# Kernel optimization log

Measured on AMD Instinct MI355X. Metric: run time of the kernel, lower is better.

Reference implementation:

```python
import jax, jax.numpy as jnp
import numpy as np

B, S, F_IN, D, H, DFF, L = 64, 256, 64, 512, 8, 2048, 6
A_DIM, FEAT, OUT = 8, 32, 5
EPS = 1e-3  # keras default epsilon for BatchNorm/LayerNorm


def _sinusoidal_pes(seq_len, d_model):
    pos = np.arange(seq_len)[:, None].astype(np.float32)
    i = np.arange(d_model)[None, :].astype(np.float32)
    angle = pos / np.power(10000.0, (2.0 * np.floor(i / 2.0)) / d_model)
    pe = np.zeros((seq_len, d_model), dtype=np.float32)
    pe[:, 0::2] = np.sin(angle[:, 0::2])
    pe[:, 1::2] = np.cos(angle[:, 1::2])
    return jnp.asarray(pe)


def setup_inputs() -> dict:
    key = jax.random.key(0)
    ks = jax.random.split(key, 16)
    w = lambda k, shape: 0.02 * jax.random.normal(k, shape, dtype=jnp.float32)
    return {
        'state': jax.random.normal(ks[0], (B, S, F_IN), dtype=jnp.float32),
        'action': jax.random.normal(ks[1], (B, A_DIM), dtype=jnp.float32),
        'pes': _sinusoidal_pes(S, D),
        'W_emb': w(ks[2], (F_IN, D)), 'b_emb': jnp.zeros((D,), jnp.float32),
        'Wq': w(ks[3], (L, D, D)), 'bq': jnp.zeros((L, D), jnp.float32),
        'Wk': w(ks[4], (L, D, D)), 'bk': jnp.zeros((L, D), jnp.float32),
        'Wv': w(ks[5], (L, D, D)), 'bv': jnp.zeros((L, D), jnp.float32),
        'Wo': w(ks[6], (L, D, D)), 'bo': jnp.zeros((L, D), jnp.float32),
        'bn_gamma': jnp.ones((L, D), jnp.float32), 'bn_beta': jnp.zeros((L, D), jnp.float32),
        'W1': w(ks[7], (L, D, DFF)), 'b1': jnp.zeros((L, DFF), jnp.float32),
        'W2': w(ks[8], (L, DFF, D)), 'b2': jnp.zeros((L, D), jnp.float32),
        'ln_gamma': jnp.ones((L, D), jnp.float32), 'ln_beta': jnp.zeros((L, D), jnp.float32),
        'Wf': w(ks[9], (S * D, FEAT)), 'bf': jnp.zeros((FEAT,), jnp.float32),
        'Wfin': w(ks[10], (FEAT + A_DIM, OUT)), 'bfin': jnp.zeros((OUT,), jnp.float32),
    }


def _encoder(x, pes, layer_params):
    # x: [B, S, D]
    x = x + pes  # positional encoding

    def step(h, p):
        Wq, bq, Wk, bk, Wv, bv, Wo, bo, gb, bb, W1, b1, W2, b2, gl, bl = p
        b, s, d = h.shape
        dh = d // H
        q = (h @ Wq + bq).reshape(b, s, H, dh)
        k = (h @ Wk + bk).reshape(b, s, H, dh)
        v = (h @ Wv + bv).reshape(b, s, H, dh)
        scores = jnp.einsum('bqhd,bkhd->bhqk', q, k) / jnp.sqrt(jnp.asarray(dh, h.dtype))
        attn = jax.nn.softmax(scores, axis=-1)
        ctx = jnp.einsum('bhqk,bkhd->bqhd', attn, v).reshape(b, s, d)
        ctx = ctx @ Wo + bo
        y = h + ctx
        # BatchNormalization over (batch, seq), per-channel (training-mode batch stats)
        mu = y.mean(axis=(0, 1))
        var = y.var(axis=(0, 1))
        y = gb * (y - mu) * jax.lax.rsqrt(var + EPS) + bb
        # FFN + residual + LayerNorm
        f = jax.nn.relu(y @ W1 + b1) @ W2 + b2
        z = y + f
        mu2 = z.mean(axis=-1, keepdims=True)
        var2 = z.var(axis=-1, keepdims=True)
        z = gl * (z - mu2) * jax.lax.rsqrt(var2 + EPS) + bl
        return z, None

    x, _ = jax.lax.scan(step, x, layer_params)
    return x


def reference(state, action, pes, W_emb, b_emb, Wq, bq, Wk, bk, Wv, bv, Wo, bo,
              bn_gamma, bn_beta, W1, b1, W2, b2, ln_gamma, ln_beta, Wf, bf, Wfin, bfin):
    x = state @ W_emb + b_emb                       # [B, S, D]
    layer_params = (Wq, bq, Wk, bk, Wv, bv, Wo, bo, bn_gamma, bn_beta,
                    W1, b1, W2, b2, ln_gamma, ln_beta)
    enc = _encoder(x, pes, layer_params)            # [B, S, D]
    flat = enc.reshape(enc.shape[0], -1)            # [B, S*D]
    feat = flat @ Wf + bf                           # [B, 32]
    out = jnp.concatenate([feat, action], axis=-1) @ Wfin + bfin  # [B, 5]
    return out
```

## Files before the change

kernel.cpp:

```cpp
#include <hip/hip_runtime.h>

typedef short bf16x8 __attribute__((ext_vector_type(8)));
typedef float f32x4 __attribute__((ext_vector_type(4)));
typedef unsigned short us;

#define BN_EPS 1e-3f

static __device__ __forceinline__ us f2bs(float x) {
  unsigned int u = __builtin_bit_cast(unsigned int, x);
  unsigned int r = (u + 0x7FFFu + ((u >> 16) & 1u)) >> 16;
  return (us)r;
}
static __device__ __forceinline__ float b2f(us v) {
  unsigned int u = (unsigned int)v << 16;
  return __builtin_bit_cast(float, u);
}

static __device__ __forceinline__ void gl_lds16(const us* g, us* l) {
  __builtin_amdgcn_global_load_lds(
      (const __attribute__((address_space(1))) void*)g,
      (__attribute__((address_space(3))) void*)l, 16, 0, 0);
}

__global__ __launch_bounds__(256) void transpose_bf16(
    const float* __restrict__ src, us* __restrict__ dst, int K, int N,
    long sstride, long dstride) {
  long sbs = (long)blockIdx.z * sstride;
  long sbd = (long)blockIdx.z * dstride;
  __shared__ float tile[32][33];
  int tx = threadIdx.x & 31, ty = threadIdx.x >> 5;
  int k0 = blockIdx.x * 32, n0 = blockIdx.y * 32;
  for (int i = 0; i < 32; i += 8)
    tile[ty + i][tx] = src[sbs + (long)(k0 + ty + i) * N + n0 + tx];
  __syncthreads();
  for (int i = 0; i < 32; i += 8)
    dst[sbd + (long)(n0 + ty + i) * K + k0 + tx] = f2bs(tile[tx][ty + i]);
}

__global__ __launch_bounds__(256) void embed_kernel(
    const float* __restrict__ state, const float* __restrict__ Wemb,
    const float* __restrict__ bemb, const float* __restrict__ pes,
    us* __restrict__ hb) {
  int t = threadIdx.x;
  int row0 = blockIdx.x * 8;
  __shared__ float st[8][64];
  {
    int i = t;
    st[i >> 6][i & 63] = state[(long)row0 * 64 + i];
    i += 256;
    st[i >> 6][i & 63] = state[(long)row0 * 64 + i];
  }
  __syncthreads();
  int c0 = t, c1 = t + 256;
  float acc0[8], acc1[8];
#pragma unroll
  for (int r = 0; r < 8; ++r) { acc0[r] = 0.f; acc1[r] = 0.f; }
  for (int kk = 0; kk < 64; ++kk) {
    float w0 = Wemb[kk * 512 + c0], w1 = Wemb[kk * 512 + c1];
#pragma unroll
    for (int r = 0; r < 8; ++r) {
      acc0[r] += st[r][kk] * w0;
      acc1[r] += st[r][kk] * w1;
    }
  }
  float be0 = bemb[c0], be1 = bemb[c1];
#pragma unroll
  for (int r = 0; r < 8; ++r) {
    int row = row0 + r, s = row & 255;
    hb[(long)row * 512 + c0] = f2bs(acc0[r] + be0 + pes[(long)s * 512 + c0]);
    hb[(long)row * 512 + c1] = f2bs(acc1[r] + be1 + pes[(long)s * 512 + c1]);
  }
}

enum { EPI_QKV = 0, EPI_RESID_BF16 = 1, EPI_RELU_BF16 = 2, EPI_FFN2_BF16 = 3,
       EPI_FEAT = 4 };

template <int EPI>
__global__ __launch_bounds__(512, 2) void gemm256(
    const us* __restrict__ A, int lda, const us* __restrict__ Bt, int ldb,
    void* __restrict__ Cout, void* __restrict__ C2, void* __restrict__ C3,
    int ldc, const float* __restrict__ bias, const us* __restrict__ resid,
    const float* __restrict__ gamma, const float* __restrict__ beta, int K) {
  const int tid = threadIdx.x;
  const int w = tid >> 6, l = tid & 63;
  const int wr = w >> 2, wc = w & 3;
  const int lr = l & 15, lh = l >> 4;
  const long m0 = (long)blockIdx.x * 256;
  const long n0 = (long)blockIdx.y * 256;
  const int KC = K >> 5;
  __shared__ __align__(16) us sh[4 * 16384];
  const int o = tid * 16;
  const int lg = o ^ ((o >> 2) & 0x30);
  const int sr = lg >> 6;
  const int sc = (lg & 63) >> 1;
  const int pb = lr * 32 + ((lh * 8) ^ ((lr & 3) << 3));
  const us* Asl = sh + wr * 4096 + pb;
  const us* Bsl = sh + 8192 + (wc >> 1) * 4096 + (wc & 1) * 2048 + pb;

  for (int j = 0; j < 3; ++j) {
    us* slot = sh + j * 16384;
    gl_lds16(A + (m0 + sr) * lda + j * 32 + sc, slot + tid * 8);
    gl_lds16(A + (m0 + 128 + sr) * lda + j * 32 + sc, slot + 4096 + tid * 8);
    gl_lds16(Bt + (n0 + sr) * ldb + j * 32 + sc, slot + 8192 + tid * 8);
    gl_lds16(Bt + (n0 + 128 + sr) * ldb + j * 32 + sc, slot + 12288 + tid * 8);
  }
  asm volatile("s_waitcnt vmcnt(8)" ::: "memory");
  __builtin_amdgcn_s_barrier();

  f32x4 acc[8][4] = {};
  for (int c = 0; c < KC; ++c) {
    const int soff = (c & 3) * 16384;
    const bool st = (c + 3) < KC;
    us* nslot = sh + ((c + 3) & 3) * 16384;
    const int nk = (c + 3) * 32;
    if (st) {
      gl_lds16(A + (m0 + sr) * lda + nk + sc, nslot + tid * 8);
      gl_lds16(A + (m0 + 128 + sr) * lda + nk + sc, nslot + 4096 + tid * 8);
    }
    bf16x8 bfr[4], af[4];
#pragma unroll
    for (int ni = 0; ni < 4; ++ni)
      bfr[ni] = *(const bf16x8*)(Bsl + soff + ni * 512);
#pragma unroll
    for (int mi = 0; mi < 4; ++mi)
      af[mi] = *(const bf16x8*)(Asl + soff + mi * 512);
    __builtin_amdgcn_s_barrier();
    __builtin_amdgcn_s_setprio(1);
#pragma unroll
    for (int mi = 0; mi < 4; ++mi)
#pragma unroll
      for (int ni = 0; ni < 4; ++ni)
        acc[mi][ni] = __builtin_amdgcn_mfma_f32_16x16x32_bf16(
            af[mi], bfr[ni], acc[mi][ni], 0, 0, 0);
    __builtin_amdgcn_s_setprio(0);
    __builtin_amdgcn_s_barrier();
    if (st) {
      gl_lds16(Bt + (n0 + sr) * ldb + nk + sc, nslot + 8192 + tid * 8);
      gl_lds16(Bt + (n0 + 128 + sr) * ldb + nk + sc, nslot + 12288 + tid * 8);
    }
#pragma unroll
    for (int mi = 0; mi < 4; ++mi)
      af[mi] = *(const bf16x8*)(Asl + soff + (mi + 4) * 512);
    __builtin_amdgcn_s_barrier();
    __builtin_amdgcn_s_setprio(1);
#pragma unroll
    for (int mi = 0; mi < 4; ++mi)
#pragma unroll
      for (int ni = 0; ni < 4; ++ni)
        acc[mi + 4][ni] = __builtin_amdgcn_mfma_f32_16x16x32_bf16(
            af[mi], bfr[ni], acc[mi + 4][ni], 0, 0, 0);
    __builtin_amdgcn_s_setprio(0);
    if (c < KC - 3)
      asm volatile("s_waitcnt vmcnt(8)" ::: "memory");
    else if (c == KC - 3)
      asm volatile("s_waitcnt vmcnt(4)" ::: "memory");
    else if (c == KC - 2)
      asm volatile("s_waitcnt vmcnt(0)" ::: "memory");
    __builtin_amdgcn_s_barrier();
  }
#pragma unroll
  for (int mi = 0; mi < 8; ++mi)
#pragma unroll
    for (int ni = 0; ni < 4; ++ni) {
      const int cl = wc * 64 + ni * 16 + lr;
      const float bv_ = bias[(int)n0 + cl];
#pragma unroll
      for (int q_ = 0; q_ < 4; ++q_) {
        const int rl = wr * 128 + mi * 16 + lh * 4 + q_;
        sh[rl * 256 + cl] = f2bs(fmaxf(acc[mi][ni][q_] + bv_, 0.f));
      }
    }
  asm volatile("s_waitcnt lgkmcnt(0)" ::: "memory");
  __builtin_amdgcn_s_barrier();
  for (int i = tid; i < 8192; i += 512) {
    const int idx = i * 8;
    const int row = idx >> 8, col = idx & 255;
    *(uint4*)&((us*)Cout)[(m0 + row) * ldc + n0 + col] = *(uint4*)&sh[idx];
  }
  (void)resid; (void)C2; (void)C3; (void)gamma; (void)beta;
}

__global__ __launch_bounds__(512, 2) void gemm256x128_ffn2(
    const us* __restrict__ A, int lda, const us* __restrict__ Bt, int ldb,
    us* __restrict__ Cout, int ldc, const float* __restrict__ bias,
    const us* __restrict__ resid, const float* __restrict__ gsA,
    const float* __restrict__ gsB, int K) {
  const int tid = threadIdx.x;
  const int w = tid >> 6, l = tid & 63;
  const int wr = w >> 1, wc = w & 1;
  const int lr = l & 15, lh = l >> 4;
  const long m0 = (long)blockIdx.x * 256;
  const long n0 = (long)blockIdx.y * 128;
  const int KC = K >> 5;
  __shared__ __align__(16) us sh[4 * 12288];
  const int o = tid * 16;
  const int lg = o ^ ((o >> 2) & 0x30);
  const int sr = lg >> 6;
  const int sc = (lg & 63) >> 1;
  const int pb = lr * 32 + ((lh * 8) ^ ((lr & 3) << 3));
  const us* Asl = sh + wr * 2048 + pb;
  const us* Bsl = sh + 8192 + wc * 2048 + pb;

  for (int j = 0; j < 3; ++j) {
    us* slot = sh + j * 12288;
    gl_lds16(A + (m0 + sr) * lda + j * 32 + sc, slot + tid * 8);
    gl_lds16(A + (m0 + 128 + sr) * lda + j * 32 + sc, slot + 4096 + tid * 8);
    gl_lds16(Bt + (n0 + sr) * ldb + j * 32 + sc, slot + 8192 + tid * 8);
  }
  asm volatile("s_waitcnt vmcnt(6)" ::: "memory");
  __builtin_amdgcn_s_barrier();

  f32x4 acc[4][4] = {};
  for (int c = 0; c < KC; ++c) {
    const int soff = (c & 3) * 12288;
    const bool st = (c + 3) < KC;
    us* nslot = sh + ((c + 3) & 3) * 12288;
    const int nk = (c + 3) * 32;
    if (st) {
      gl_lds16(A + (m0 + sr) * lda + nk + sc, nslot + tid * 8);
      gl_lds16(A + (m0 + 128 + sr) * lda + nk + sc, nslot + 4096 + tid * 8);
    }
    bf16x8 bfr[4], af[2];
#pragma unroll
    for (int ni = 0; ni < 4; ++ni)
      bfr[ni] = *(const bf16x8*)(Bsl + soff + ni * 512);
#pragma unroll
    for (int mi = 0; mi < 2; ++mi)
      af[mi] = *(const bf16x8*)(Asl + soff + mi * 512);
    __builtin_amdgcn_s_barrier();
    __builtin_amdgcn_s_setprio(1);
#pragma unroll
    for (int mi = 0; mi < 2; ++mi)
#pragma unroll
      for (int ni = 0; ni < 4; ++ni)
        acc[mi][ni] = __builtin_amdgcn_mfma_f32_16x16x32_bf16(
            af[mi], bfr[ni], acc[mi][ni], 0, 0, 0);
    __builtin_amdgcn_s_setprio(0);
    __builtin_amdgcn_s_barrier();
    if (st) {
      gl_lds16(Bt + (n0 + sr) * ldb + nk + sc, nslot + 8192 + tid * 8);
    }
#pragma unroll
    for (int mi = 0; mi < 2; ++mi)
      af[mi] = *(const bf16x8*)(Asl + soff + (mi + 2) * 512);
    __builtin_amdgcn_s_barrier();
    __builtin_amdgcn_s_setprio(1);
#pragma unroll
    for (int mi = 0; mi < 2; ++mi)
#pragma unroll
      for (int ni = 0; ni < 4; ++ni)
        acc[mi + 2][ni] = __builtin_amdgcn_mfma_f32_16x16x32_bf16(
            af[mi], bfr[ni], acc[mi + 2][ni], 0, 0, 0);
    __builtin_amdgcn_s_setprio(0);
    if (c < KC - 3)
      asm volatile("s_waitcnt vmcnt(6)" ::: "memory");
    else if (c == KC - 3)
      asm volatile("s_waitcnt vmcnt(3)" ::: "memory");
    else if (c == KC - 2)
      asm volatile("s_waitcnt vmcnt(0)" ::: "memory");
    __builtin_amdgcn_s_barrier();
  }
#pragma unroll
  for (int mi = 0; mi < 4; ++mi)
#pragma unroll
    for (int ni = 0; ni < 4; ++ni) {
      const int cl = wc * 64 + ni * 16 + lr;
      const int col = (int)n0 + cl;
      const float bv_ = bias[col];
      const float aa = gsA[col], bb2 = gsB[col];
#pragma unroll
      for (int q_ = 0; q_ < 4; ++q_) {
        const int rl = wr * 64 + mi * 16 + lh * 4 + q_;
        float ybn = b2f(resid[(m0 + rl) * ldc + col]) * aa + bb2;
        sh[rl * 128 + cl] = f2bs(ybn + acc[mi][ni][q_] + bv_);
      }
    }
  asm volatile("s_waitcnt lgkmcnt(0)" ::: "memory");
  __builtin_amdgcn_s_barrier();
  for (int i = tid; i < 4096; i += 512) {
    const int idx = i * 8;
    const int row = idx >> 7, col = idx & 127;
    *(uint4*)&Cout[(m0 + row) * ldc + n0 + col] = *(uint4*)&sh[idx];
  }
}

template <int BM, int BN, int WM, int WN, int EPI>
__global__ __launch_bounds__((BM / WM) * (BN / WN) * 64)
void gemm_bt(const us* __restrict__ A, int lda, long batchA,
             const us* __restrict__ Bt, int ldb, long batchB,
             void* __restrict__ Cout, void* __restrict__ C2,
             void* __restrict__ C3, int ldc,
             const float* __restrict__ bias,
             const us* __restrict__ resid,
             float* __restrict__ gsum, float* __restrict__ gsumsq,
             const float* __restrict__ gamma, const float* __restrict__ beta,
             int K) {
  constexpr int WCols = BN / WN;
  constexpr int NT = (BM / WM) * (BN / WN) * 64;
  constexpr int NW = NT / 64;
  constexpr int MI = WM / 16, NI = WN / 16;
  constexpr int LA = BM / 8;
  constexpr int LB = BN / 8;
  const int tid = threadIdx.x;
  const int w = tid >> 6, l = tid & 63;
  const int wr = w / WCols, wc = w % WCols;
  const int lr = l & 15, lh = l >> 4;
  const int z = blockIdx.z;
  const long m0 = (long)blockIdx.x * BM;
  const long n0 = (long)blockIdx.y * BN;
  A += (long)z * batchA;
  Bt += (long)z * batchB;
  __shared__ __align__(16) us smem[BM * 64 + BN * 64];
  us* Asm = smem;
  us* Bsm = smem + BM * 64;
  const int srow = l >> 3, scol = (l & 7) << 3;
  f32x4 acc[MI][NI] = {};
  for (int kt = 0; kt < K; kt += 64) {
    __syncthreads();
    for (int j = w; j < LA; j += NW) {
      int rb = j * 8;
      gl_lds16(A + (m0 + rb + srow) * lda + kt + scol, Asm + rb * 64);
    }
    for (int j = w; j < LB; j += NW) {
      int rb = j * 8;
      gl_lds16(Bt + (n0 + rb + srow) * ldb + kt + scol, Bsm + rb * 64);
    }
    asm volatile("s_waitcnt vmcnt(0)" ::: "memory");
    __syncthreads();
#pragma unroll
    for (int kk = 0; kk < 64; kk += 32) {
      bf16x8 af[MI], bfr[NI];
#pragma unroll
      for (int mi = 0; mi < MI; ++mi)
        af[mi] = *(const bf16x8*)&Asm[(wr * WM + mi * 16 + lr) * 64 + kk + lh * 8];
#pragma unroll
      for (int ni = 0; ni < NI; ++ni)
        bfr[ni] = *(const bf16x8*)&Bsm[(wc * WN + ni * 16 + lr) * 64 + kk + lh * 8];
#pragma unroll
      for (int mi = 0; mi < MI; ++mi)
#pragma unroll
        for (int ni = 0; ni < NI; ++ni)
          acc[mi][ni] = __builtin_amdgcn_mfma_f32_16x16x32_bf16(
              af[mi], bfr[ni], acc[mi][ni], 0, 0, 0);
    }
  }

  if constexpr (EPI == EPI_QKV) {
    const int seg = (int)(n0 >> 9);
    const int nc0 = (int)(n0 & 511);
    if (seg == 2) {
#pragma unroll
      for (int mi = 0; mi < MI; ++mi) {
#pragma unroll
        for (int ni = 0; ni < NI; ++ni) {
          const int segc = nc0 + wc * WN + ni * 16 + lr;
          const float bv_ = beta[segc];
          ushort4 pv;
#pragma unroll
          for (int q_ = 0; q_ < 4; ++q_)
            ((us*)&pv)[q_] = f2bs(acc[mi][ni][q_] + bv_);
          const long row0g = m0 + wr * WM + mi * 16 + lh * 4;
          const long oo = (((row0g >> 8) * 8 + (segc >> 6)) * 64 + (segc & 63)) *
                              256 + (row0g & 255);
          *(ushort4*)&((us*)C3)[oo] = pv;
        }
      }
    } else {
      __syncthreads();
#pragma unroll
      for (int mi = 0; mi < MI; ++mi)
#pragma unroll
        for (int ni = 0; ni < NI; ++ni) {
          const int cl = wc * WN + ni * 16 + lr;
          const float bv_ = seg == 0 ? bias[nc0 + cl] : gamma[nc0 + cl];
#pragma unroll
          for (int q_ = 0; q_ < 4; ++q_) {
            const int rl = wr * WM + mi * 16 + lh * 4 + q_;
            smem[rl * BN + cl] = f2bs(acc[mi][ni][q_] + bv_);
          }
        }
      __syncthreads();
      us* dstp = seg == 0 ? (us*)Cout : (us*)C2;
      for (int i = tid; i < (BM * BN) / 8; i += NT) {
        const int idx = i * 8;
        const int row = idx / BN, colc = idx % BN;
        *(uint4*)&dstp[(m0 + row) * 512 + nc0 + colc] = *(uint4*)&smem[idx];
      }
    }
  } else if constexpr (EPI == EPI_RESID_BF16 && BM == 128 && BN == 128) {
    __syncthreads();
    float cs[NI] = {}, cq[NI] = {};
#pragma unroll
    for (int mi = 0; mi < MI; ++mi)
#pragma unroll
      for (int ni = 0; ni < NI; ++ni) {
        const int cl = wc * WN + ni * 16 + lr;
        const int col = (int)n0 + cl;
        const float bv_ = bias[col];
#pragma unroll
        for (int q_ = 0; q_ < 4; ++q_) {
          const int rl = wr * WM + mi * 16 + lh * 4 + q_;
          float v = acc[mi][ni][q_] + bv_ + b2f(resid[(m0 + rl) * ldc + col]);
          cs[ni] += v;
          cq[ni] += v * v;
          smem[rl * BN + cl] = f2bs(v);
        }
      }
#pragma unroll
    for (int ni = 0; ni < NI; ++ni) {
      float s = cs[ni], qv = cq[ni];
      s += __shfl_xor(s, 16);
      qv += __shfl_xor(qv, 16);
      s += __shfl_xor(s, 32);
      qv += __shfl_xor(qv, 32);
      if (lh == 0) {
        const int col = (int)n0 + wc * WN + ni * 16 + lr;
        atomicAdd(&gsum[col], s);
        atomicAdd(&gsumsq[col], qv);
      }
    }
    __syncthreads();
    for (int i = tid; i < (BM * BN) / 8; i += NT) {
      const int idx = i * 8;
      const int row = idx / BN, colc = idx % BN;
      *(uint4*)&((us*)Cout)[(m0 + row) * ldc + n0 + colc] = *(uint4*)&smem[idx];
    }
  } else {
#pragma unroll
    for (int mi = 0; mi < MI; ++mi) {
#pragma unroll
      for (int ni = 0; ni < NI; ++ni) {
        const int col = (int)n0 + wc * WN + ni * 16 + lr;
#pragma unroll
        for (int q_ = 0; q_ < 4; ++q_) {
          const long row = m0 + wr * WM + mi * 16 + lh * 4 + q_;
          if constexpr (EPI == EPI_FEAT) {
            atomicAdd(&((float*)Cout)[row * ldc + col], acc[mi][ni][q_]);
          }
        }
      }
    }
  }
}

__global__ __launch_bounds__(256) void attn_kernel(
    const us* __restrict__ q, const us* __restrict__ k,
    const us* __restrict__ vt, us* __restrict__ ctx) {
  const int half = blockIdx.x;
  const int z = blockIdx.y;
  const int b = z >> 3, hh = z & 7;
  const long qkBase = (long)b * 131072 + hh * 64;
  const int tid = threadIdx.x, w = tid >> 6, l = tid & 63;
  const int lr = l & 15, lh = l >> 4;
  __shared__ __align__(16) us Qs[32][72];
  __shared__ __align__(16) us Ks[64][72];
  __shared__ __align__(16) us Pb[32][264];
  __shared__ float fred[32][2];
  const int qr = (w >> 1) * 16, qc = (w & 1) * 32;
  const us* vb = vt + (long)z * 16384;
  const int ldr = tid >> 3, ldc = (tid & 7) << 3;

  for (int qi = 0; qi < 4; ++qi) {
    const int qb = half * 4 + qi;
    *(uint4*)&Qs[ldr][ldc] =
        *(const uint4*)(q + qkBase + (long)(qb * 32 + ldr) * 512 + ldc);
    f32x4 sacc[4][2] = {};
    for (int skb = 0; skb < 4; ++skb) {
      __syncthreads();
      for (int i = tid; i < 512; i += 256) {
        int r = i >> 3, c = (i & 7) << 3;
        *(uint4*)&Ks[r][c] =
            *(const uint4*)(k + qkBase + (long)(skb * 64 + r) * 512 + c);
      }
      __syncthreads();
#pragma unroll
      for (int kh = 0; kh < 2; ++kh) {
        bf16x8 aq = *(const bf16x8*)&Qs[qr + lr][kh * 32 + lh * 8];
#pragma unroll
        for (int ni = 0; ni < 2; ++ni) {
          bf16x8 bkk = *(const bf16x8*)&Ks[qc + ni * 16 + lr][kh * 32 + lh * 8];
          sacc[skb][ni] = __builtin_amdgcn_mfma_f32_16x16x32_bf16(
              aq, bkk, sacc[skb][ni], 0, 0, 0);
        }
      }
    }
    float m0[4] = {-1e30f, -1e30f, -1e30f, -1e30f};
#pragma unroll
    for (int skb = 0; skb < 4; ++skb)
#pragma unroll
      for (int ni = 0; ni < 2; ++ni)
#pragma unroll
        for (int q_ = 0; q_ < 4; ++q_) {
          float v = sacc[skb][ni][q_] * 0.125f;
          sacc[skb][ni][q_] = v;
          m0[q_] = fmaxf(m0[q_], v);
        }
#pragma unroll
    for (int off = 1; off < 16; off <<= 1)
#pragma unroll
      for (int q_ = 0; q_ < 4; ++q_)
        m0[q_] = fmaxf(m0[q_], __shfl_xor(m0[q_], off));
    if (lr == 0) {
#pragma unroll
      for (int q_ = 0; q_ < 4; ++q_) fred[qr + lh * 4 + q_][w & 1] = m0[q_];
    }
    __syncthreads();
#pragma unroll
    for (int q_ = 0; q_ < 4; ++q_) {
      int row = qr + lh * 4 + q_;
      m0[q_] = fmaxf(fred[row][0], fred[row][1]);
    }
    float s0[4] = {0.f, 0.f, 0.f, 0.f};
#pragma unroll
    for (int skb = 0; skb < 4; ++skb)
#pragma unroll
      for (int ni = 0; ni < 2; ++ni)
#pragma unroll
        for (int q_ = 0; q_ < 4; ++q_) {
          float e = __expf(sacc[skb][ni][q_] - m0[q_]);
          sacc[skb][ni][q_] = e;
          s0[q_] += e;
        }
#pragma unroll
    for (int off = 1; off < 16; off <<= 1)
#pragma unroll
      for (int q_ = 0; q_ < 4; ++q_) s0[q_] += __shfl_xor(s0[q_], off);
    __syncthreads();
    if (lr == 0) {
#pragma unroll
      for (int q_ = 0; q_ < 4; ++q_) fred[qr + lh * 4 + q_][w & 1] = s0[q_];
    }
    __syncthreads();
#pragma unroll
    for (int q_ = 0; q_ < 4; ++q_) {
      int row = qr + lh * 4 + q_;
      s0[q_] = 1.f / (fred[row][0] + fred[row][1]);
    }
#pragma unroll
    for (int skb = 0; skb < 4; ++skb)
#pragma unroll
      for (int ni = 0; ni < 2; ++ni)
#pragma unroll
        for (int q_ = 0; q_ < 4; ++q_)
          Pb[qr + lh * 4 + q_][skb * 64 + qc + ni * 16 + lr] =
              f2bs(sacc[skb][ni][q_] * s0[q_]);
    f32x4 pacc[2] = {};
    for (int kc = 0; kc < 256; kc += 64) {
      __syncthreads();
      for (int i = tid; i < 512; i += 256) {
        int r = i >> 3, c = (i & 7) << 3;
        *(uint4*)&Ks[r][c] = *(const uint4*)(vb + (long)r * 256 + kc + c);
      }
      __syncthreads();
#pragma unroll
      for (int kh = 0; kh < 2; ++kh) {
        bf16x8 ap = *(const bf16x8*)&Pb[qr + lr][kc + kh * 32 + lh * 8];
#pragma unroll
        for (int ni = 0; ni < 2; ++ni) {
          bf16x8 bv2 = *(const bf16x8*)&Ks[qc + ni * 16 + lr][kh * 32 + lh * 8];
          pacc[ni] = __builtin_amdgcn_mfma_f32_16x16x32_bf16(
              ap, bv2, pacc[ni], 0, 0, 0);
        }
      }
    }
    const long cb2 = ((long)(b * 256 + qb * 32)) * 512 + hh * 64;
#pragma unroll
    for (int ni = 0; ni < 2; ++ni)
#pragma unroll
      for (int q_ = 0; q_ < 4; ++q_) {
        int row = qr + lh * 4 + q_;
        int col = qc + ni * 16 + lr;
        ctx[cb2 + (long)row * 512 + col] = f2bs(pacc[ni][q_]);
      }
  }
}

__global__ void bn_coef(float* __restrict__ gsum, float* __restrict__ gsumsq,
                        const float* __restrict__ gamma,
                        const float* __restrict__ beta) {
  int c = blockIdx.x * 256 + threadIdx.x;
  if (c < 512) {
    const float invN = 1.f / 16384.f;
    float mu = gsum[c] * invN;
    float var = gsumsq[c] * invN - mu * mu;
    float a = gamma[c] * rsqrtf(var + BN_EPS);
    float b = beta[c] - mu * a;
    gsum[c] = a;
    gsumsq[c] = b;
  }
}

__global__ __launch_bounds__(256) void fold_w1(
    const us* __restrict__ W1T, const float* __restrict__ aa,
    const float* __restrict__ bb, const float* __restrict__ b1,
    us* __restrict__ W1s, float* __restrict__ bias1f) {
  int n = blockIdx.x * 4 + (threadIdx.x >> 6);
  int l = threadIdx.x & 63;
  int k0 = l * 8;
  const us* row = W1T + (long)n * 512;
  us tmp[8], outv[8];
  *(uint4*)tmp = *(const uint4*)(row + k0);
  float dot = 0.f;
#pragma unroll
  for (int j = 0; j < 8; ++j) {
    float wv = b2f(tmp[j]);
    dot += bb[k0 + j] * wv;
    outv[j] = f2bs(aa[k0 + j] * wv);
  }
  *(uint4*)(W1s + (long)n * 512 + k0) = *(uint4*)outv;
  for (int off = 32; off >= 1; off >>= 1) dot += __shfl_down(dot, off);
  if (l == 0) bias1f[n] = b1[n] + dot;
}

__global__ __launch_bounds__(128) void ln_kernel(
    const us* __restrict__ zin, const float* __restrict__ g,
    const float* __restrict__ b, us* __restrict__ hb,
    float* __restrict__ gsum, float* __restrict__ gsumsq) {
  int r = blockIdx.x, t = threadIdx.x;
  if (r == 0) {
    for (int i = t; i < 512; i += 128) {
      gsum[i] = 0.f;
      gsumsq[i] = 0.f;
    }
  }
  const us* zr = zin + (long)r * 512;
  ushort4 vz = *(const ushort4*)(zr + t * 4);
  float v0 = b2f(((us*)&vz)[0]), v1 = b2f(((us*)&vz)[1]);
  float v2 = b2f(((us*)&vz)[2]), v3 = b2f(((us*)&vz)[3]);
  float s = v0 + v1 + v2 + v3;
  float qs = v0 * v0 + v1 * v1 + v2 * v2 + v3 * v3;
  for (int off = 32; off >= 1; off >>= 1) {
    s += __shfl_down(s, off);
    qs += __shfl_down(qs, off);
  }
  __shared__ float ls[2], lq[2];
  if ((t & 63) == 0) {
    ls[t >> 6] = s;
    lq[t >> 6] = qs;
  }
  __syncthreads();
  float mu = (ls[0] + ls[1]) * (1.f / 512.f);
  float var = (lq[0] + lq[1]) * (1.f / 512.f) - mu * mu;
  float rs = rsqrtf(var + BN_EPS);
  float4 gg = *(const float4*)(g + t * 4);
  float4 bb = *(const float4*)(b + t * 4);
  ushort4 hv;
  ((us*)&hv)[0] = f2bs(gg.x * (v0 - mu) * rs + bb.x);
  ((us*)&hv)[1] = f2bs(gg.y * (v1 - mu) * rs + bb.y);
  ((us*)&hv)[2] = f2bs(gg.z * (v2 - mu) * rs + bb.z);
  ((us*)&hv)[3] = f2bs(gg.w * (v3 - mu) * rs + bb.w);
  *(ushort4*)(hb + (long)r * 512 + t * 4) = hv;
}

__global__ void zerof(float* __restrict__ p, int n) {
  int i = blockIdx.x * 256 + threadIdx.x;
  if (i < n) p[i] = 0.f;
}

__global__ __launch_bounds__(320) void final_head(
    const float* __restrict__ feat, const float* __restrict__ bf_,
    const float* __restrict__ action, const float* __restrict__ Wfin,
    const float* __restrict__ bfin, float* __restrict__ out) {
  int t = threadIdx.x;
  int b = t & 63, o = t >> 6;
  float acc = bfin[o];
  for (int j = 0; j < 32; ++j) acc += (feat[b * 32 + j] + bf_[j]) * Wfin[j * 5 + o];
  for (int j = 0; j < 8; ++j) acc += action[b * 8 + j] * Wfin[(32 + j) * 5 + o];
  out[b * 5 + o] = acc;
}

extern "C" void kernel_launch(void* const* d_in, const int* in_sizes, int n_in,
                              void* d_out, int out_size, void* d_ws,
                              size_t ws_size, hipStream_t stream) {
  const float* state = (const float*)d_in[0];
  const float* action = (const float*)d_in[1];
  const float* pes = (const float*)d_in[2];
  const float* W_emb = (const float*)d_in[3];
  const float* b_emb = (const float*)d_in[4];
  const float* Wq = (const float*)d_in[5];
  const float* bq = (const float*)d_in[6];
  const float* Wk = (const float*)d_in[7];
  const float* bk = (const float*)d_in[8];
  const float* Wv = (const float*)d_in[9];
  const float* bv = (const float*)d_in[10];
  const float* Wo = (const float*)d_in[11];
  const float* bo = (const float*)d_in[12];
  const float* bn_g = (const float*)d_in[13];
  const float* bn_b = (const float*)d_in[14];
  const float* W1 = (const float*)d_in[15];
  const float* b1 = (const float*)d_in[16];
  const float* W2 = (const float*)d_in[17];
  const float* b2 = (const float*)d_in[18];
  const float* ln_g = (const float*)d_in[19];
  const float* ln_b = (const float*)d_in[20];
  const float* Wf = (const float*)d_in[21];
  const float* bf_ = (const float*)d_in[22];
  const float* Wfin = (const float*)d_in[23];
  const float* bfin = (const float*)d_in[24];
  float* out = (float*)d_out;
  (void)in_sizes; (void)n_in; (void)out_size;

  char* wp = (char*)d_ws;
  size_t off = 0;
  auto take = [&](size_t bytes) {
    void* p = wp + off;
    off += (bytes + 255) & ~(size_t)255;
    return p;
  };
  us* qkvT = (us*)take(6ull * 1536 * 512 * 2);
  us* WoT = (us*)take(6ull * 512 * 512 * 2);
  us* W1T = (us*)take(6ull * 2048 * 512 * 2);
  us* W2T = (us*)take(6ull * 512 * 2048 * 2);
  us* WfT = (us*)take(32ull * 131072 * 2);
  us* hb = (us*)take(16384ull * 512 * 2);
  us* ybf = (us*)take(16384ull * 512 * 2);
  us* W1s = (us*)take(2048ull * 512 * 2);
  float* bias1f = (float*)take(2048 * 4);
  us* qb_ = (us*)take(16384ull * 512 * 2);
  us* kb_ = (us*)take(16384ull * 512 * 2);
  us* vt = (us*)take(16384ull * 512 * 2);
  us* bigR4 = (us*)take(33554432ull * 2);
  float* gsum = (float*)take(512 * 4);
  float* gsumsq = (float*)take(512 * 4);
  float* feat = (float*)take(2048 * 4);
  us* ctxb = bigR4;
  us* f1 = bigR4;
  us* zbf = qb_;

  if (off > ws_size) return;

  transpose_bf16<<<dim3(16, 16, 6), 256, 0, stream>>>(Wq, qkvT, 512, 512,
                                                      262144, 786432);
  transpose_bf16<<<dim3(16, 16, 6), 256, 0, stream>>>(Wk, qkvT + 262144, 512,
                                                      512, 262144, 786432);
  transpose_bf16<<<dim3(16, 16, 6), 256, 0, stream>>>(Wv, qkvT + 524288, 512,
                                                      512, 262144, 786432);
  transpose_bf16<<<dim3(16, 16, 6), 256, 0, stream>>>(Wo, WoT, 512, 512,
                                                      262144, 262144);
  transpose_bf16<<<dim3(16, 64, 6), 256, 0, stream>>>(W1, W1T, 512, 2048,
                                                      1048576, 1048576);
  transpose_bf16<<<dim3(64, 16, 6), 256, 0, stream>>>(W2, W2T, 2048, 512,
                                                      1048576, 1048576);
  transpose_bf16<<<dim3(4096, 1, 1), 256, 0, stream>>>(Wf, WfT, 131072, 32,
                                                       0, 0);
  embed_kernel<<<2048, 256, 0, stream>>>(state, W_emb, b_emb, pes, hb);
  zerof<<<4, 256, 0, stream>>>(gsum, 1024);

  for (int l = 0; l < 6; ++l) {
    const us* qkvTl = qkvT + (size_t)l * 786432;
    const us* WoTl = WoT + (size_t)l * 262144;
    const us* W1Tl = W1T + (size_t)l * 1048576;
    const us* W2Tl = W2T + (size_t)l * 1048576;

    gemm_bt<128, 128, 64, 64, EPI_QKV><<<dim3(128, 12, 1), 256, 0, stream>>>(
        hb, 512, 0, qkvTl, 512, 0, qb_, kb_, vt, 512, bq + l * 512,
        nullptr, nullptr, nullptr, bk + l * 512, bv + l * 512, 512);
    attn_kernel<<<dim3(2, 512), 256, 0, stream>>>(qb_, kb_, vt, ctxb);
    gemm_bt<128, 128, 64, 64, EPI_RESID_BF16><<<dim3(128, 4, 1), 256, 0, stream>>>(
        ctxb, 512, 0, WoTl, 512, 0, ybf, nullptr, nullptr, 512, bo + l * 512,
        hb, gsum, gsumsq, nullptr, nullptr, 512);
    bn_coef<<<2, 256, 0, stream>>>(gsum, gsumsq, bn_g + l * 512,
                                   bn_b + l * 512);
    fold_w1<<<512, 256, 0, stream>>>(W1Tl, gsum, gsumsq, b1 + l * 2048, W1s,
                                     bias1f);
    gemm256<EPI_RELU_BF16><<<dim3(64, 8), 512, 0, stream>>>(
        ybf, 512, W1s, 512, f1, nullptr, nullptr, 2048, bias1f, nullptr,
        nullptr, nullptr, 512);
    gemm256x128_ffn2<<<dim3(64, 4), 512, 0, stream>>>(
        f1, 2048, W2Tl, 2048, zbf, 512, b2 + l * 512, ybf, gsum, gsumsq, 2048);
    ln_kernel<<<16384, 128, 0, stream>>>(zbf, ln_g + l * 512, ln_b + l * 512,
                                         hb, gsum, gsumsq);
  }

  zerof<<<8, 256, 0, stream>>>(feat, 2048);
  gemm_bt<64, 32, 32, 16, EPI_FEAT><<<dim3(1, 1, 128), 256, 0, stream>>>(
      hb, 131072, 1024, WfT, 131072, 1024, feat, nullptr, nullptr, 32,
      nullptr, nullptr, nullptr, nullptr, nullptr, nullptr, 1024);
  final_head<<<1, 320, 0, stream>>>(feat, bf_, action, Wfin, bfin, out);
}
```

Baseline: 1.432 ms.

## Stage full K and V per head in LDS and process all queries per block

The attention kernel now runs one 512-thread block per (batch, head) instead of two 256-thread blocks. Each block loads the whole 256-row K and V for the head into shared memory once, instead of reloading K and V tiles for every 32-query chunk. This removes redundant global loads and many per-chunk barriers. In exchange, shared memory per block grows to roughly 80 KB and the grid halves to 512 blocks, which may lower occupancy and reduce latency hiding.

```diff
diff --git a/kernel.cpp b/kernel.cpp
--- a/kernel.cpp
+++ b/kernel.cpp
@@ -443,47 +443,54 @@
   }
 }
 
-__global__ __launch_bounds__(256) void attn_kernel(
+__global__ __launch_bounds__(512) void attn_kernel(
     const us* __restrict__ q, const us* __restrict__ k,
     const us* __restrict__ vt, us* __restrict__ ctx) {
-  const int half = blockIdx.x;
-  const int z = blockIdx.y;
+  const int z = blockIdx.x;
   const int b = z >> 3, hh = z & 7;
   const long qkBase = (long)b * 131072 + hh * 64;
   const int tid = threadIdx.x, w = tid >> 6, l = tid & 63;
   const int lr = l & 15, lh = l >> 4;
-  __shared__ __align__(16) us Qs[32][72];
-  __shared__ __align__(16) us Ks[64][72];
-  __shared__ __align__(16) us Pb[32][264];
-  __shared__ float fred[32][2];
-  const int qr = (w >> 1) * 16, qc = (w & 1) * 32;
+  const int hf = w >> 2, w2 = w & 3;
+  const int qr = (w2 >> 1) * 16, qc = (w2 & 1) * 32;
+  __shared__ __align__(16) us Kf[256][72];
+  __shared__ __align__(16) us Vf[64][264];
+  __shared__ __align__(16) us Qs[2][32][72];
+  __shared__ __align__(16) us Pb[2][32][264];
+  __shared__ float fred[2][32][2];
   const us* vb = vt + (long)z * 16384;
-  const int ldr = tid >> 3, ldc = (tid & 7) << 3;
+  for (int i = tid; i < 2048; i += 512) {
+    int r = i >> 3, c = (i & 7) << 3;
+    *(uint4*)&Kf[r][c] = *(const uint4*)(k + qkBase + (long)r * 512 + c);
+  }
+  for (int i = tid; i < 2048; i += 512) {
+    int r = i >> 5, c = (i & 31) << 3;
+    *(uint4*)&Vf[r][c] = *(const uint4*)(vb + (long)r * 256 + c);
+  }
+  const int th = tid & 255, qhf = tid >> 8;
+  const int qlr = th >> 3, qlc = (th & 7) << 3;
+  __syncthreads();
 
   for (int qi = 0; qi < 4; ++qi) {
-    const int qb = half * 4 + qi;
-    *(uint4*)&Qs[ldr][ldc] =
-        *(const uint4*)(q + qkBase + (long)(qb * 32 + ldr) * 512 + ldc);
+    const int qbl = qi * 2 + qhf;
+    *(uint4*)&Qs[qhf][qlr][qlc] =
+        *(const uint4*)(q + qkBase + (long)(qbl * 32 + qlr) * 512 + qlc);
+    __syncthreads();
+    const int myqb = qi * 2 + hf;
     f32x4 sacc[4][2] = {};
-    for (int skb = 0; skb < 4; ++skb) {
-      __syncthreads();
-      for (int i = tid; i < 512; i += 256) {
-        int r = i >> 3, c = (i & 7) << 3;
-        *(uint4*)&Ks[r][c] =
-            *(const uint4*)(k + qkBase + (long)(skb * 64 + r) * 512 + c);
-      }
-      __syncthreads();
+#pragma unroll
+    for (int skb = 0; skb < 4; ++skb)
 #pragma unroll
       for (int kh = 0; kh < 2; ++kh) {
-        bf16x8 aq = *(const bf16x8*)&Qs[qr + lr][kh * 32 + lh * 8];
+        bf16x8 aq = *(const bf16x8*)&Qs[hf][qr + lr][kh * 32 + lh * 8];
 #pragma unroll
         for (int ni = 0; ni < 2; ++ni) {
-          bf16x8 bkk = *(const bf16x8*)&Ks[qc + ni * 16 + lr][kh * 32 + lh * 8];
+          bf16x8 bkk =
+              *(const bf16x8*)&Kf[skb * 64 + qc + ni * 16 + lr][kh * 32 + lh * 8];
           sacc[skb][ni] = __builtin_amdgcn_mfma_f32_16x16x32_bf16(
               aq, bkk, sacc[skb][ni], 0, 0, 0);
         }
       }
-    }
     float m0[4] = {-1e30f, -1e30f, -1e30f, -1e30f};
 #pragma unroll
     for (int skb = 0; skb < 4; ++skb)
@@ -502,13 +509,14 @@
         m0[q_] = fmaxf(m0[q_], __shfl_xor(m0[q_], off));
     if (lr == 0) {
 #pragma unroll
-      for (int q_ = 0; q_ < 4; ++q_) fred[qr + lh * 4 + q_][w & 1] = m0[q_];
+      for (int q_ = 0; q_ < 4; ++q_)
+        fred[hf][qr + lh * 4 + q_][w2 & 1] = m0[q_];
     }
     __syncthreads();
 #pragma unroll
     for (int q_ = 0; q_ < 4; ++q_) {
       int row = qr + lh * 4 + q_;
-      m0[q_] = fmaxf(fred[row][0], fred[row][1]);
+      m0[q_] = fmaxf(fred[hf][row][0], fred[hf][row][1]);
     }
     float s0[4] = {0.f, 0.f, 0.f, 0.f};
 #pragma unroll
@@ -528,13 +536,14 @@
     __syncthreads();
     if (lr == 0) {
 #pragma unroll
-      for (int q_ = 0; q_ < 4; ++q_) fred[qr + lh * 4 + q_][w & 1] = s0[q_];
+      for (int q_ = 0; q_ < 4; ++q_)
+        fred[hf][qr + lh * 4 + q_][w2 & 1] = s0[q_];
     }
     __syncthreads();
 #pragma unroll
     for (int q_ = 0; q_ < 4; ++q_) {
       int row = qr + lh * 4 + q_;
-      s0[q_] = 1.f / (fred[row][0] + fred[row][1]);
+      s0[q_] = 1.f / (fred[hf][row][0] + fred[hf][row][1]);
     }
 #pragma unroll
     for (int skb = 0; skb < 4; ++skb)
@@ -542,28 +551,24 @@
       for (int ni = 0; ni < 2; ++ni)
 #pragma unroll
         for (int q_ = 0; q_ < 4; ++q_)
-          Pb[qr + lh * 4 + q_][skb * 64 + qc + ni * 16 + lr] =
+          Pb[hf][qr + lh * 4 + q_][skb * 64 + qc + ni * 16 + lr] =
               f2bs(sacc[skb][ni][q_] * s0[q_]);
+    __syncthreads();
     f32x4 pacc[2] = {};
-    for (int kc = 0; kc < 256; kc += 64) {
-      __syncthreads();
-      for (int i = tid; i < 512; i += 256) {
-        int r = i >> 3, c = (i & 7) << 3;
-        *(uint4*)&Ks[r][c] = *(const uint4*)(vb + (long)r * 256 + kc + c);
-      }
-      __syncthreads();
+#pragma unroll
+    for (int kc = 0; kc < 256; kc += 64)
 #pragma unroll
       for (int kh = 0; kh < 2; ++kh) {
-        bf16x8 ap = *(const bf16x8*)&Pb[qr + lr][kc + kh * 32 + lh * 8];
+        bf16x8 ap = *(const bf16x8*)&Pb[hf][qr + lr][kc + kh * 32 + lh * 8];
 #pragma unroll
         for (int ni = 0; ni < 2; ++ni) {
-          bf16x8 bv2 = *(const bf16x8*)&Ks[qc + ni * 16 + lr][kh * 32 + lh * 8];
+          bf16x8 bv2 =
+              *(const bf16x8*)&Vf[qc + ni * 16 + lr][kc + kh * 32 + lh * 8];
           pacc[ni] = __builtin_amdgcn_mfma_f32_16x16x32_bf16(
               ap, bv2, pacc[ni], 0, 0, 0);
         }
       }
-    }
-    const long cb2 = ((long)(b * 256 + qb * 32)) * 512 + hh * 64;
+    const long cb2 = ((long)(b * 256 + myqb * 32)) * 512 + hh * 64;
 #pragma unroll
     for (int ni = 0; ni < 2; ++ni)
 #pragma unroll
@@ -572,6 +577,7 @@
         int col = qc + ni * 16 + lr;
         ctx[cb2 + (long)row * 512 + col] = f2bs(pacc[ni][q_]);
       }
+    __syncthreads();
   }
 }
 
@@ -755,7 +761,7 @@
     gemm_bt<128, 128, 64, 64, EPI_QKV><<<dim3(128, 12, 1), 256, 0, stream>>>(
         hb, 512, 0, qkvTl, 512, 0, qb_, kb_, vt, 512, bq + l * 512,
         nullptr, nullptr, nullptr, bk + l * 512, bv + l * 512, 512);
-    attn_kernel<<<dim3(2, 512), 256, 0, stream>>>(qb_, kb_, vt, ctxb);
+    attn_kernel<<<512, 512, 0, stream>>>(qb_, kb_, vt, ctxb);
     gemm_bt<128, 128, 64, 64, EPI_RESID_BF16><<<dim3(128, 4, 1), 256, 0, stream>>>(
         ctxb, 512, 0, WoTl, 512, 0, ybf, nullptr, nullptr, 512, bo + l * 512,
         hb, gsum, gsumsq, nullptr, nullptr, 512);
```

Result: faster. 1.377 ms (-3.9%).
